# Optimization experiments

Hardware: AMD Instinct MI355X
Metric: run time of the kernel (lower is better)

Reference implementation:

```python
import jax, jax.numpy as jnp
import numpy as np

B, S, D, H = 2, 2048, 2048, 16
HD = D // H          # head_dim = 128
FF = 8192            # intermediate_size
LN_EPS = 1e-05
BIT_EPS = 1e-05


def _rope_tables(seq_len, head_dim):
    inv_freq = 1.0 / (10000.0 ** (np.arange(0, head_dim, 2, dtype=np.float64) / head_dim))
    ang = np.arange(seq_len, dtype=np.float64)[:, None] * inv_freq[None, :]  # [S, HD/2]
    ang = np.concatenate([ang, ang], axis=-1)  # [S, HD]
    return jnp.asarray(np.cos(ang), jnp.float32), jnp.asarray(np.sin(ang), jnp.float32)


def setup_inputs() -> dict:
    key = jax.random.key(0)
    ks = jax.random.split(key, 9)
    hidden_states = jax.random.normal(ks[0], (B, S, D), jnp.float32)
    # causal additive mask [1, S, S]
    causal = jnp.tril(jnp.ones((S, S), bool))
    attention_mask = jnp.where(causal, 0.0, -1e9)[None].astype(jnp.float32)
    cos, sin = _rope_tables(S, HD)
    w = lambda k, o, i: jax.random.normal(k, (o, i), jnp.float32) * 0.02
    return {
        'hidden_states': hidden_states,
        'attention_mask': attention_mask,
        'cos': cos, 'sin': sin,
        'wq': w(ks[1], D, D), 'wk': w(ks[2], D, D),
        'wv': w(ks[3], D, D), 'wo': w(ks[4], D, D),
        'wg': w(ks[5], FF, D), 'wu': w(ks[6], FF, D), 'wd': w(ks[7], D, FF),
        'ln1_w': jnp.ones((D,), jnp.float32),
        'ln2_w': jnp.ones((D,), jnp.float32),
    }


def bitlinear(x, w):
    # ternarize: clamp(round(w / (mean|w| + eps)), -1, 1); int8 cast in torch
    # breaks grad through the ternary values -> stop_gradient here.
    scale = jnp.mean(jnp.abs(w))
    tern = jax.lax.stop_gradient(jnp.clip(jnp.round(w / (scale + BIT_EPS)), -1.0, 1.0))
    # dequant = ternary * mean|w|, then standard linear (x @ W^T)
    return jnp.einsum('bsi,oi->bso', x, tern * scale)


def rmsnorm(x, w, eps=LN_EPS):
    var = jnp.mean(jnp.square(x.astype(jnp.float32)), axis=-1, keepdims=True)
    return w * (x * jax.lax.rsqrt(var + eps))


def rotate_half(x):
    x1, x2 = jnp.split(x, 2, axis=-1)
    return jnp.concatenate([-x2, x1], axis=-1)


def apply_rope(q, k, cos, sin):
    # q, k: [B, S, D] -> per-head rope -> back to [B, S, D]
    qh = q.reshape(B, S, H, HD)
    kh = k.reshape(B, S, H, HD)
    c = cos[None, :, None, :]
    s = sin[None, :, None, :]
    qe = qh * c + rotate_half(qh) * s
    ke = kh * c + rotate_half(kh) * s
    return qe.reshape(B, S, D), ke.reshape(B, S, D)


def reference(hidden_states, attention_mask, cos, sin,
              wq, wk, wv, wo, wg, wu, wd, ln1_w, ln2_w):
    residual = hidden_states
    # --- attention block ---
    x = rmsnorm(hidden_states, ln1_w)
    q = bitlinear(x, wq)
    k = bitlinear(x, wk)
    v = bitlinear(x, wv)
    q, k = apply_rope(q, k, cos, sin)
    # NOTE: scores over FULL hidden dim (no head split), scaled by sqrt(head_dim),
    # exactly as in the original module.
    scores = jnp.einsum('bsd,btd->bst', q, k) / jnp.sqrt(jnp.float32(HD))
    scores = scores + attention_mask
    probs = jax.nn.softmax(scores, axis=-1)
    attn_out = jnp.einsum('bst,btd->bsd', probs, v)
    attn_out = bitlinear(attn_out, wo)
    h = residual + attn_out
    # --- MLP block ---
    residual = h
    y = rmsnorm(h, ln2_w)
    gated = bitlinear(y, wg) * bitlinear(y, wu)
    out = bitlinear(gated, wd)
    return residual + out
```

## Files before the change

kernel.cpp:

```cpp
#include <hip/hip_runtime.h>
#include <stdint.h>

#define DEV __device__ __forceinline__

typedef __attribute__((ext_vector_type(8))) short short8;
typedef __attribute__((ext_vector_type(8))) __bf16 bf16x8;
typedef __attribute__((ext_vector_type(4))) float f32x4;

DEV unsigned short f2bf(float f) {
  union { float f; unsigned int u; } v; v.f = f;
  unsigned int r = v.u + 0x7fffu + ((v.u >> 16) & 1u);
  return (unsigned short)(r >> 16);
}
DEV float bf2f(unsigned short h) {
  union { unsigned int u; float f; } v; v.u = ((unsigned int)h) << 16;
  return v.f;
}
DEV f32x4 mfma16(short8 a, short8 b, f32x4 c) {
  return __builtin_amdgcn_mfma_f32_16x16x32_bf16(
      __builtin_bit_cast(bf16x8, a), __builtin_bit_cast(bf16x8, b), c, 0, 0, 0);
}
DEV void gload_lds16(const void* g, void* lds) {
  __builtin_amdgcn_global_load_lds(
      (const __attribute__((address_space(1))) void*)g,
      (__attribute__((address_space(3))) void*)lds, 16, 0, 0);
}

struct MArgs {
  const float* src[7];
  unsigned short* dst[7];
  int n[7];
  int sidx[7];
};

__global__ __launch_bounds__(256) void absmean_partial_multi(
    MArgs a, float* __restrict__ partial) {
  const int m = blockIdx.y;
  const float4* w4 = (const float4*)a.src[m];
  const int n4 = a.n[m] >> 2;
  float s = 0.f;
  for (int i = blockIdx.x * 256 + threadIdx.x; i < n4; i += 1024 * 256) {
    float4 v = w4[i];
    s += fabsf(v.x) + fabsf(v.y) + fabsf(v.z) + fabsf(v.w);
  }
#pragma unroll
  for (int mm = 1; mm < 64; mm <<= 1) s += __shfl_xor(s, mm);
  __shared__ float red[4];
  if ((threadIdx.x & 63) == 0) red[threadIdx.x >> 6] = s;
  __syncthreads();
  if (threadIdx.x == 0)
    partial[m * 1024 + blockIdx.x] = red[0] + red[1] + red[2] + red[3];
}

__global__ __launch_bounds__(256) void absmean_final(
    const float* __restrict__ partial, float* __restrict__ scales) {
  __shared__ double red[256];
  const int m = blockIdx.x;
  double s = 0.0;
  for (int i = threadIdx.x; i < 1024; i += 256) s += (double)partial[m * 1024 + i];
  red[threadIdx.x] = s;
  __syncthreads();
  for (int t = 128; t > 0; t >>= 1) {
    if (threadIdx.x < t) red[threadIdx.x] += red[threadIdx.x + t];
    __syncthreads();
  }
  if (threadIdx.x == 0) {
    const long long cnt = (m < 4) ? 4194304ll : 16777216ll;
    scales[m] = (float)(red[0] / (double)cnt);
  }
}

__global__ __launch_bounds__(256) void quantize_multi(
    MArgs a, const float* __restrict__ scales) {
  const int m = blockIdx.y;
  const float sc = scales[a.sidx[m]];
  const float inv = 1.f / (sc + 1e-5f);
  const float4* src = (const float4*)a.src[m];
  ushort4* dst = (ushort4*)a.dst[m];
  const int n4 = a.n[m] >> 2;
  for (int i = blockIdx.x * 256 + threadIdx.x; i < n4; i += 2048 * 256) {
    float4 v = src[i];
    ushort4 o;
    o.x = f2bf(fminf(fmaxf(rintf(v.x * inv), -1.f), 1.f) * sc);
    o.y = f2bf(fminf(fmaxf(rintf(v.y * inv), -1.f), 1.f) * sc);
    o.z = f2bf(fminf(fmaxf(rintf(v.z * inv), -1.f), 1.f) * sc);
    o.w = f2bf(fminf(fmaxf(rintf(v.w * inv), -1.f), 1.f) * sc);
    dst[i] = o;
  }
}

__global__ __launch_bounds__(256) void rmsnorm_k(
    const float* __restrict__ x, const float* __restrict__ wt,
    unsigned short* __restrict__ out) {
  const long long t = blockIdx.x;
  const float* xr = x + t * 2048;
  const int i0 = threadIdx.x * 8;
  float4 a = *(const float4*)(xr + i0);
  float4 b = *(const float4*)(xr + i0 + 4);
  float ss = a.x * a.x + a.y * a.y + a.z * a.z + a.w * a.w +
             b.x * b.x + b.y * b.y + b.z * b.z + b.w * b.w;
#pragma unroll
  for (int m = 1; m < 64; m <<= 1) ss += __shfl_xor(ss, m);
  __shared__ float red[4];
  if ((threadIdx.x & 63) == 0) red[threadIdx.x >> 6] = ss;
  __syncthreads();
  float tot = red[0] + red[1] + red[2] + red[3];
  float rs = rsqrtf(tot * (1.f / 2048.f) + 1e-5f);
  float4 wa = *(const float4*)(wt + i0);
  float4 wb = *(const float4*)(wt + i0 + 4);
  ushort4 o1, o2;
  o1.x = f2bf(a.x * wa.x * rs); o1.y = f2bf(a.y * wa.y * rs);
  o1.z = f2bf(a.z * wa.z * rs); o1.w = f2bf(a.w * wa.w * rs);
  o2.x = f2bf(b.x * wb.x * rs); o2.y = f2bf(b.y * wb.y * rs);
  o2.z = f2bf(b.z * wb.z * rs); o2.w = f2bf(b.w * wb.w * rs);
  *(ushort4*)(out + t * 2048 + i0) = o1;
  *(ushort4*)(out + t * 2048 + i0 + 4) = o2;
}

__global__ __launch_bounds__(256) void rope_k(
    const unsigned short* __restrict__ qkv, const float* __restrict__ cosT,
    const float* __restrict__ sinT, unsigned short* __restrict__ qr,
    unsigned short* __restrict__ kr, unsigned short* __restrict__ vt) {
  const long long gid = (long long)blockIdx.x * 256 + threadIdx.x;
  const int t = (int)(gid >> 10);
  const int r = (int)(gid & 1023);
  const int h = r >> 6, d = r & 63;
  const int s = t & 2047, b = t >> 11;
  const unsigned short* row = qkv + (long long)t * 6144;
  const float c = cosT[s * 128 + d], sn = sinT[s * 128 + d];
  const int col = h * 128 + d;
  const float SC = 0.08838834764831845f;
  float q1 = bf2f(row[col]), q2 = bf2f(row[col + 64]);
  float k1 = bf2f(row[2048 + col]), k2 = bf2f(row[2048 + col + 64]);
  long long ob = (long long)t * 2048 + col;
  qr[ob] = f2bf((q1 * c - q2 * sn) * SC);
  qr[ob + 64] = f2bf((q2 * c + q1 * sn) * SC);
  kr[ob] = f2bf(k1 * c - k2 * sn);
  kr[ob + 64] = f2bf(k2 * c + k1 * sn);
  vt[((long long)b * 2048 + col) * 2048 + s] = row[4096 + col];
  vt[((long long)b * 2048 + col + 64) * 2048 + s] = row[4096 + col + 64];
}

__global__ __launch_bounds__(256) void softmax_causal(
    const float* __restrict__ scores, unsigned short* __restrict__ probs) {
  const int r = blockIdx.x;
  const int s = r & 2047;
  const float* src = scores + (long long)r * 2048;
  unsigned short* dst = probs + (long long)r * 2048;
  const int L = s + 1;
  const int j0 = threadIdx.x * 8;
  float4 a = *(const float4*)(src + j0);
  float4 b = *(const float4*)(src + j0 + 4);
  float v[8] = {a.x, a.y, a.z, a.w, b.x, b.y, b.z, b.w};
  float mx = -1e30f;
#pragma unroll
  for (int i = 0; i < 8; ++i) {
    if (j0 + i >= L) v[i] = -1e30f;
    mx = fmaxf(mx, v[i]);
  }
#pragma unroll
  for (int m = 1; m < 64; m <<= 1) mx = fmaxf(mx, __shfl_xor(mx, m));
  __shared__ float redM[4], redS[4];
  if ((threadIdx.x & 63) == 0) redM[threadIdx.x >> 6] = mx;
  __syncthreads();
  mx = fmaxf(fmaxf(redM[0], redM[1]), fmaxf(redM[2], redM[3]));
  float sum = 0.f;
#pragma unroll
  for (int i = 0; i < 8; ++i) {
    v[i] = (j0 + i < L) ? __expf(v[i] - mx) : 0.f;
    sum += v[i];
  }
#pragma unroll
  for (int m = 1; m < 64; m <<= 1) sum += __shfl_xor(sum, m);
  if ((threadIdx.x & 63) == 0) redS[threadIdx.x >> 6] = sum;
  __syncthreads();
  const float inv = 1.f / (redS[0] + redS[1] + redS[2] + redS[3]);
  ushort4 o1, o2;
  o1.x = f2bf(v[0] * inv); o1.y = f2bf(v[1] * inv);
  o1.z = f2bf(v[2] * inv); o1.w = f2bf(v[3] * inv);
  o2.x = f2bf(v[4] * inv); o2.y = f2bf(v[5] * inv);
  o2.z = f2bf(v[6] * inv); o2.w = f2bf(v[7] * inv);
  *(ushort4*)(dst + j0) = o1;
  *(ushort4*)(dst + j0 + 4) = o2;
}

template <int EPI, int CAUSAL>
__global__ __launch_bounds__(512, 2) void gemm256(
    const unsigned short* __restrict__ A, const unsigned short* __restrict__ Bw,
    void* __restrict__ Cp, const void* __restrict__ Ep,
    int N, int K, int nbx, int kLen, int ngTot,
    long long sAz, long long sBz, long long zCout) {
  __shared__ __align__(16) unsigned short lds[4 * 2 * 8192];
  __shared__ __align__(16) unsigned short ldsDummy[512];
  const int tid = threadIdx.x;
  const int wid = tid >> 6, l = tid & 63;
  const int wr = wid >> 2, wcn = wid & 3;

  const int nwg = gridDim.x;
  const int q8 = nwg >> 3;
  const int lin = (blockIdx.x & 7) * q8 + (blockIdx.x >> 3);
  const int t32 = lin >> 5, r32 = lin & 31;
  const int tpr = nbx >> 3;
  const int tm = t32 / tpr, tn = t32 - tm * tpr;
  const long long m0 = (long long)(tm * 4 + (r32 >> 3)) * 256;
  const long long n0 = (long long)(tn * 8 + (r32 & 7)) * 256;
  if (CAUSAL == 1 && n0 > m0) return;
  const int z = blockIdx.z;
  A += z * sAz;
  Bw += z * sBz;
  const long long kbase = (long long)z * kLen;
  const long long zofs = (long long)z * zCout;
  int ng = ngTot;
  if (CAUSAL == 2) {
    const int lim = (int)((m0 + 256) >> 5);
    ng = lim < ng ? lim : ng;
  }

  const int stRow = (l >> 2);
  const int stCol = (((l & 3) ^ ((l >> 3) & 3))) * 8;
  auto stage = [&](int chunk) {
    if (chunk < ng) {
      char* base = (char*)lds + ((chunk & 3) * 2) * 16384;
      const long long kcol = kbase + (long long)chunk * 32 + stCol;
#pragma unroll
      for (int i = 0; i < 2; ++i) {
        const int row = (wid * 2 + i) * 16 + stRow;
        gload_lds16(&A[(m0 + row) * K + kcol], base + (wid * 2 + i) * 1024);
        gload_lds16(&Bw[(n0 + row) * K + kcol],
                    base + 16384 + (wid * 2 + i) * 1024);
      }
    } else {
#pragma unroll
      for (int i = 0; i < 4; ++i) gload_lds16(&A[m0 * K], (char*)ldsDummy);
    }
  };

  const int ar = l & 15;
  const int rj = ((l >> 4) ^ ((l >> 1) & 3)) << 4;

  auto readA03 = [&](int slot, short8 (&a)[4]) {
    const char* sA = (const char*)lds + (slot * 2) * 16384;
#pragma unroll
    for (int m = 0; m < 4; ++m)
      a[m] = *(const short8*)(sA + (wr * 128 + m * 16 + ar) * 64 + rj);
  };
  auto readA47 = [&](int slot, short8 (&a)[4]) {
    const char* sA = (const char*)lds + (slot * 2) * 16384;
#pragma unroll
    for (int m = 0; m < 4; ++m)
      a[m] = *(const short8*)(sA + (wr * 128 + (m + 4) * 16 + ar) * 64 + rj);
  };
  auto readB = [&](int slot, short8 (&b)[4]) {
    const char* sB = (const char*)lds + (slot * 2 + 1) * 16384;
#pragma unroll
    for (int n = 0; n < 4; ++n)
      b[n] = *(const short8*)(sB + (wcn * 64 + n * 16 + ar) * 64 + rj);
  };

  f32x4 acc[8][4] = {};
  short8 aX[4], bX[4], aY[4], bY[4], a47[4];

  stage(0); stage(1); stage(2);
  asm volatile("s_waitcnt vmcnt(4)" ::: "memory");
  __builtin_amdgcn_s_barrier();
  readA03(0, aX);
  readB(0, bX);

  auto chunkBody = [&](int c, bool sync, short8 (&cur03)[4], short8 (&curB)[4],
                       short8 (&nxt03)[4], short8 (&nxtB)[4]) {
    const int slot = c & 3;
    readA47(slot, a47);
    stage(c + 3);
    __builtin_amdgcn_s_setprio(1);
#pragma unroll
    for (int m = 0; m < 4; ++m)
#pragma unroll
      for (int n = 0; n < 4; ++n)
        acc[m][n] = mfma16(cur03[m], curB[n], acc[m][n]);
    __builtin_amdgcn_s_setprio(0);
    if (sync) {
      asm volatile("s_waitcnt vmcnt(4)" ::: "memory");
      __builtin_amdgcn_s_barrier();
    }
    readA03((c + 1) & 3, nxt03);
    readB((c + 1) & 3, nxtB);
    __builtin_amdgcn_s_setprio(1);
#pragma unroll
    for (int m = 0; m < 4; ++m)
#pragma unroll
      for (int n = 0; n < 4; ++n)
        acc[m + 4][n] = mfma16(a47[m], curB[n], acc[m + 4][n]);
    __builtin_amdgcn_s_setprio(0);
  };

  for (int c = 0; c < ng; c += 2) {
    chunkBody(c, false, aX, bX, aY, bY);
    chunkBody(c + 1, true, aY, bY, aX, bX);
  }
  asm volatile("s_waitcnt vmcnt(0)" ::: "memory");
  __builtin_amdgcn_s_barrier();

  const int orow = (l >> 4) * 4, ocol = l & 15;
#pragma unroll
  for (int m = 0; m < 8; ++m)
#pragma unroll
    for (int n = 0; n < 4; ++n)
#pragma unroll
      for (int r = 0; r < 4; ++r) {
        const long long gr = m0 + wr * 128 + m * 16 + orow + r;
        const long long gc = n0 + wcn * 64 + n * 16 + ocol;
        const long long idx = zofs + gr * N + gc;
        const float v = acc[m][n][r];
        if (EPI == 0) {
          ((unsigned short*)Cp)[idx] = f2bf(v);
        } else if (EPI == 2) {
          ((unsigned short*)Cp)[idx] = f2bf(bf2f(((const unsigned short*)Ep)[idx]) * v);
        } else {
          ((float*)Cp)[idx] = v;
        }
      }
}

__global__ __launch_bounds__(256) void combine2(
    const float* __restrict__ ep, const float* __restrict__ p,
    float* __restrict__ out, long long n4) {
  const float4* e4 = (const float4*)ep;
  const float4* p4 = (const float4*)p;
  float4* o4 = (float4*)out;
  for (long long i = blockIdx.x * 256 + threadIdx.x; i < n4; i += 2048 * 256) {
    float4 a = e4[i], b = p4[i], c = p4[i + n4];
    float4 o;
    o.x = a.x + b.x + c.x; o.y = a.y + b.y + c.y;
    o.z = a.z + b.z + c.z; o.w = a.w + b.w + c.w;
    o4[i] = o;
  }
}

extern "C" void kernel_launch(void* const* d_in, const int* in_sizes, int n_in,
                              void* d_out, int out_size, void* d_ws, size_t ws_size,
                              hipStream_t stream) {
  (void)in_sizes; (void)n_in; (void)out_size; (void)ws_size;
  const float* hidden = (const float*)d_in[0];
  const float* cosT = (const float*)d_in[2];
  const float* sinT = (const float*)d_in[3];
  const float* wq = (const float*)d_in[4];
  const float* wk = (const float*)d_in[5];
  const float* wv = (const float*)d_in[6];
  const float* wo = (const float*)d_in[7];
  const float* wg = (const float*)d_in[8];
  const float* wu = (const float*)d_in[9];
  const float* wd = (const float*)d_in[10];
  const float* ln1 = (const float*)d_in[11];
  const float* ln2 = (const float*)d_in[12];

  const size_t MB = 1ull << 20;
  char* ws = (char*)d_ws;
  unsigned short* xn    = (unsigned short*)(ws + 0);
  unsigned short* wqkvq = (unsigned short*)(ws + 16 * MB);
  unsigned short* qkv   = (unsigned short*)(ws + 40 * MB);
  unsigned short* qrb   = (unsigned short*)(ws + 88 * MB);
  unsigned short* krb   = (unsigned short*)(ws + 104 * MB);
  unsigned short* vtb   = (unsigned short*)(ws + 120 * MB);
  float*          scoresB = (float*)(ws + 0);
  unsigned short* probsB  = (unsigned short*)(ws + 40 * MB);
  float*          part   = (float*)(ws + 0);
  unsigned short* wgq   = (unsigned short*)(ws + 0);
  unsigned short* wuq   = (unsigned short*)(ws + 32 * MB);
  unsigned short* gbuf  = (unsigned short*)(ws + 64 * MB);
  unsigned short* attnb = (unsigned short*)(ws + 136 * MB);
  unsigned short* woq   = (unsigned short*)(ws + 152 * MB);
  float*          hbuf  = (float*)(ws + 160 * MB);
  unsigned short* ybuf  = (unsigned short*)(ws + 192 * MB);
  unsigned short* gated = (unsigned short*)(ws + 208 * MB);
  unsigned short* wdq   = (unsigned short*)(ws + 272 * MB);
  float* wspart         = (float*)(ws + 304 * MB);
  float* scales         = (float*)(ws + 304 * MB + 32768);

  MArgs am;
  am.src[0] = wq; am.src[1] = wk; am.src[2] = wv; am.src[3] = wo;
  am.src[4] = wg; am.src[5] = wu; am.src[6] = wd;
  am.n[0] = am.n[1] = am.n[2] = am.n[3] = 4194304;
  am.n[4] = am.n[5] = am.n[6] = 16777216;
  for (int i = 0; i < 7; ++i) { am.dst[i] = nullptr; am.sidx[i] = i; }
  absmean_partial_multi<<<dim3(1024, 7), 256, 0, stream>>>(am, wspart);
  absmean_final<<<7, 256, 0, stream>>>(wspart, scales);

  MArgs qe;
  qe.src[0] = wq; qe.dst[0] = wqkvq;            qe.n[0] = 4194304;  qe.sidx[0] = 0;
  qe.src[1] = wk; qe.dst[1] = wqkvq + 4194304;  qe.n[1] = 4194304;  qe.sidx[1] = 1;
  qe.src[2] = wv; qe.dst[2] = wqkvq + 8388608;  qe.n[2] = 4194304;  qe.sidx[2] = 2;
  qe.src[3] = wo; qe.dst[3] = woq;              qe.n[3] = 4194304;  qe.sidx[3] = 3;
  qe.src[4] = wd; qe.dst[4] = wdq;              qe.n[4] = 16777216; qe.sidx[4] = 6;
  qe.src[5] = wq; qe.dst[5] = nullptr; qe.n[5] = 0; qe.sidx[5] = 0;
  qe.src[6] = wq; qe.dst[6] = nullptr; qe.n[6] = 0; qe.sidx[6] = 0;
  quantize_multi<<<dim3(2048, 5), 256, 0, stream>>>(qe, scales);

  rmsnorm_k<<<4096, 256, 0, stream>>>(hidden, ln1, xn);

  gemm256<0, 0><<<dim3(384, 1, 1), 512, 0, stream>>>(
      xn, wqkvq, qkv, nullptr, 6144, 2048, 24, 2048, 64, 0, 0, 0);

  rope_k<<<16384, 256, 0, stream>>>(qkv, cosT, sinT, qrb, krb, vtb);

  gemm256<4, 1><<<dim3(64, 1, 2), 512, 0, stream>>>(
      qrb, krb, scoresB, nullptr, 2048, 2048, 8, 0, 64, 4194304, 4194304, 4194304);
  softmax_causal<<<4096, 256, 0, stream>>>(scoresB, probsB);
  gemm256<0, 2><<<dim3(64, 1, 2), 512, 0, stream>>>(
      probsB, vtb, attnb, nullptr, 2048, 2048, 8, 0, 64, 4194304, 4194304, 4194304);

  gemm256<4, 0><<<dim3(128, 1, 2), 512, 0, stream>>>(
      attnb, woq, part, nullptr, 2048, 2048, 8, 1024, 32, 0, 0, 8388608);
  combine2<<<2048, 256, 0, stream>>>(hidden, part, hbuf, 2097152);

  MArgs ql;
  ql.src[0] = wg; ql.dst[0] = wgq; ql.n[0] = 16777216; ql.sidx[0] = 4;
  ql.src[1] = wu; ql.dst[1] = wuq; ql.n[1] = 16777216; ql.sidx[1] = 5;
  for (int i = 2; i < 7; ++i) { ql.src[i] = wg; ql.dst[i] = nullptr; ql.n[i] = 0; ql.sidx[i] = 0; }
  quantize_multi<<<dim3(2048, 2), 256, 0, stream>>>(ql, scales);

  rmsnorm_k<<<4096, 256, 0, stream>>>(hbuf, ln2, ybuf);

  gemm256<0, 0><<<dim3(512, 1, 1), 512, 0, stream>>>(
      ybuf, wgq, gbuf, nullptr, 8192, 2048, 32, 2048, 64, 0, 0, 0);
  gemm256<2, 0><<<dim3(512, 1, 1), 512, 0, stream>>>(
      ybuf, wuq, gated, gbuf, 8192, 2048, 32, 2048, 64, 0, 0, 0);

  gemm256<4, 0><<<dim3(128, 1, 2), 512, 0, stream>>>(
      gated, wdq, part, nullptr, 2048, 8192, 8, 4096, 128, 0, 0, 8388608);
  combine2<<<2048, 256, 0, stream>>>(hbuf, part, (float*)d_out, 2097152);
}
```

Measured before the change: 824.8 us.

## Fuse residual combine with RMSNorm and unroll GEMM main loop by four

Replaces the separate split-K combine and second RMSNorm kernels with one kernel that sums the residual and both partials, writes h, and emits the normalized bf16 activations. This removes one launch and a re-read of the hidden buffer. The GEMM main loop is also unrolled four chunks deep so LDS slot indices and offsets become compile-time constants, which cuts address arithmetic. The unroll by four assumes ng is a multiple of four and raises code size and register pressure.

```diff
diff --git a/kernel.cpp b/kernel.cpp
--- a/kernel.cpp
+++ b/kernel.cpp
@@ -115,6 +115,48 @@
   o2.z = f2bf(b.z * wb.z * rs); o2.w = f2bf(b.w * wb.w * rs);
   *(ushort4*)(out + t * 2048 + i0) = o1;
   *(ushort4*)(out + t * 2048 + i0 + 4) = o2;
+}
+
+__global__ __launch_bounds__(256) void combine_rms(
+    const float* __restrict__ ep, const float* __restrict__ p,
+    const float* __restrict__ wt, float* __restrict__ hout,
+    unsigned short* __restrict__ yout) {
+  const long long t = blockIdx.x;
+  const int i0 = threadIdx.x * 8;
+  const long long base = t * 2048 + i0;
+  float4 e1 = *(const float4*)(ep + base);
+  float4 e2 = *(const float4*)(ep + base + 4);
+  float4 p1 = *(const float4*)(p + base);
+  float4 p2 = *(const float4*)(p + base + 4);
+  float4 q1 = *(const float4*)(p + 8388608 + base);
+  float4 q2 = *(const float4*)(p + 8388608 + base + 4);
+  float h[8] = {e1.x + p1.x + q1.x, e1.y + p1.y + q1.y,
+                e1.z + p1.z + q1.z, e1.w + p1.w + q1.w,
+                e2.x + p2.x + q2.x, e2.y + p2.y + q2.y,
+                e2.z + p2.z + q2.z, e2.w + p2.w + q2.w};
+  float4 h1 = {h[0], h[1], h[2], h[3]};
+  float4 h2 = {h[4], h[5], h[6], h[7]};
+  *(float4*)(hout + base) = h1;
+  *(float4*)(hout + base + 4) = h2;
+  float ss = 0.f;
+#pragma unroll
+  for (int i = 0; i < 8; ++i) ss += h[i] * h[i];
+#pragma unroll
+  for (int m = 1; m < 64; m <<= 1) ss += __shfl_xor(ss, m);
+  __shared__ float red[4];
+  if ((threadIdx.x & 63) == 0) red[threadIdx.x >> 6] = ss;
+  __syncthreads();
+  const float tot = red[0] + red[1] + red[2] + red[3];
+  const float rs = rsqrtf(tot * (1.f / 2048.f) + 1e-5f);
+  float4 wa = *(const float4*)(wt + i0);
+  float4 wb = *(const float4*)(wt + i0 + 4);
+  ushort4 o1, o2;
+  o1.x = f2bf(h[0] * wa.x * rs); o1.y = f2bf(h[1] * wa.y * rs);
+  o1.z = f2bf(h[2] * wa.z * rs); o1.w = f2bf(h[3] * wa.w * rs);
+  o2.x = f2bf(h[4] * wb.x * rs); o2.y = f2bf(h[5] * wb.y * rs);
+  o2.z = f2bf(h[6] * wb.z * rs); o2.w = f2bf(h[7] * wb.w * rs);
+  *(ushort4*)(yout + base) = o1;
+  *(ushort4*)(yout + base + 4) = o2;
 }
 
 __global__ __launch_bounds__(256) void rope_k(
@@ -218,9 +260,9 @@
 
   const int stRow = (l >> 2);
   const int stCol = (((l & 3) ^ ((l >> 3) & 3))) * 8;
-  auto stage = [&](int chunk) {
+  auto stage = [&](int chunk, int sslot) {
     if (chunk < ng) {
-      char* base = (char*)lds + ((chunk & 3) * 2) * 16384;
+      char* base = (char*)lds + (sslot * 2) * 16384;
       const long long kcol = kbase + (long long)chunk * 32 + stCol;
 #pragma unroll
       for (int i = 0; i < 2; ++i) {
@@ -237,66 +279,58 @@
 
   const int ar = l & 15;
   const int rj = ((l >> 4) ^ ((l >> 1) & 3)) << 4;
-
-  auto readA03 = [&](int slot, short8 (&a)[4]) {
-    const char* sA = (const char*)lds + (slot * 2) * 16384;
-#pragma unroll
-    for (int m = 0; m < 4; ++m)
-      a[m] = *(const short8*)(sA + (wr * 128 + m * 16 + ar) * 64 + rj);
-  };
-  auto readA47 = [&](int slot, short8 (&a)[4]) {
-    const char* sA = (const char*)lds + (slot * 2) * 16384;
-#pragma unroll
-    for (int m = 0; m < 4; ++m)
-      a[m] = *(const short8*)(sA + (wr * 128 + (m + 4) * 16 + ar) * 64 + rj);
-  };
-  auto readB = [&](int slot, short8 (&b)[4]) {
-    const char* sB = (const char*)lds + (slot * 2 + 1) * 16384;
-#pragma unroll
-    for (int n = 0; n < 4; ++n)
-      b[n] = *(const short8*)(sB + (wcn * 64 + n * 16 + ar) * 64 + rj);
-  };
+  const int aoff = (wr * 128 + ar) * 64 + rj;
+  const int boff = (wcn * 64 + ar) * 64 + rj;
 
   f32x4 acc[8][4] = {};
-  short8 aX[4], bX[4], aY[4], bY[4], a47[4];
-
-  stage(0); stage(1); stage(2);
+  short8 aX[4], bX[4], aY[4], bY[4];
+
+  stage(0, 0); stage(1, 1); stage(2, 2);
   asm volatile("s_waitcnt vmcnt(4)" ::: "memory");
   __builtin_amdgcn_s_barrier();
-  readA03(0, aX);
-  readB(0, bX);
-
-  auto chunkBody = [&](int c, bool sync, short8 (&cur03)[4], short8 (&curB)[4],
-                       short8 (&nxt03)[4], short8 (&nxtB)[4]) {
-    const int slot = c & 3;
-    readA47(slot, a47);
-    stage(c + 3);
-    __builtin_amdgcn_s_setprio(1);
-#pragma unroll
-    for (int m = 0; m < 4; ++m)
-#pragma unroll
-      for (int n = 0; n < 4; ++n)
-        acc[m][n] = mfma16(cur03[m], curB[n], acc[m][n]);
-    __builtin_amdgcn_s_setprio(0);
-    if (sync) {
-      asm volatile("s_waitcnt vmcnt(4)" ::: "memory");
-      __builtin_amdgcn_s_barrier();
-    }
-    readA03((c + 1) & 3, nxt03);
-    readB((c + 1) & 3, nxtB);
-    __builtin_amdgcn_s_setprio(1);
-#pragma unroll
-    for (int m = 0; m < 4; ++m)
-#pragma unroll
-      for (int n = 0; n < 4; ++n)
-        acc[m + 4][n] = mfma16(a47[m], curB[n], acc[m + 4][n]);
-    __builtin_amdgcn_s_setprio(0);
-  };
-
-  for (int c = 0; c < ng; c += 2) {
-    chunkBody(c, false, aX, bX, aY, bY);
-    chunkBody(c + 1, true, aY, bY, aX, bX);
-  }
+#pragma unroll
+  for (int m = 0; m < 4; ++m)
+    aX[m] = *(const short8*)((const char*)lds + aoff + m * 1024);
+#pragma unroll
+  for (int n = 0; n < 4; ++n)
+    bX[n] = *(const short8*)((const char*)lds + 16384 + boff + n * 1024);
+
+#define CHUNK_BODY(SLOT, NSLOT, SYNC, cur03, curB, nxt03, nxtB, cc)            \
+  {                                                                            \
+    const char* sAc = (const char*)lds + (SLOT * 2) * 16384;                   \
+    const char* sAn = (const char*)lds + (NSLOT * 2) * 16384;                  \
+    const char* sBn = (const char*)lds + (NSLOT * 2 + 1) * 16384;              \
+    short8 a47[4];                                                             \
+    _Pragma("unroll") for (int m = 0; m < 4; ++m)                              \
+        a47[m] = *(const short8*)(sAc + aoff + 4096 + m * 1024);               \
+    stage((cc) + 3, (SLOT + 3) & 3);                                           \
+    __builtin_amdgcn_s_setprio(1);                                             \
+    _Pragma("unroll") for (int m = 0; m < 4; ++m)                              \
+      _Pragma("unroll") for (int n = 0; n < 4; ++n)                            \
+          acc[m][n] = mfma16(cur03[m], curB[n], acc[m][n]);                    \
+    __builtin_amdgcn_s_setprio(0);                                             \
+    if (SYNC) {                                                                \
+      asm volatile("s_waitcnt vmcnt(4)" ::: "memory");                         \
+      __builtin_amdgcn_s_barrier();                                            \
+    }                                                                          \
+    _Pragma("unroll") for (int m = 0; m < 4; ++m)                              \
+        nxt03[m] = *(const short8*)(sAn + aoff + m * 1024);                    \
+    _Pragma("unroll") for (int n = 0; n < 4; ++n)                              \
+        nxtB[n] = *(const short8*)(sBn + boff + n * 1024);                     \
+    __builtin_amdgcn_s_setprio(1);                                             \
+    _Pragma("unroll") for (int m = 0; m < 4; ++m)                              \
+      _Pragma("unroll") for (int n = 0; n < 4; ++n)                            \
+          acc[m + 4][n] = mfma16(a47[m], curB[n], acc[m + 4][n]);              \
+    __builtin_amdgcn_s_setprio(0);                                             \
+  }
+
+  for (int c = 0; c < ng; c += 4) {
+    CHUNK_BODY(0, 1, false, aX, bX, aY, bY, c);
+    CHUNK_BODY(1, 2, true, aY, bY, aX, bX, c + 1);
+    CHUNK_BODY(2, 3, false, aX, bX, aY, bY, c + 2);
+    CHUNK_BODY(3, 0, true, aY, bY, aX, bX, c + 3);
+  }
+#undef CHUNK_BODY
   asm volatile("s_waitcnt vmcnt(0)" ::: "memory");
   __builtin_amdgcn_s_barrier();
 
@@ -410,7 +444,7 @@
 
   gemm256<4, 0><<<dim3(128, 1, 2), 512, 0, stream>>>(
       attnb, woq, part, nullptr, 2048, 2048, 8, 1024, 32, 0, 0, 8388608);
-  combine2<<<2048, 256, 0, stream>>>(hidden, part, hbuf, 2097152);
+  combine_rms<<<4096, 256, 0, stream>>>(hidden, part, ln2, hbuf, ybuf);
 
   MArgs ql;
   ql.src[0] = wg; ql.dst[0] = wgq; ql.n[0] = 16777216; ql.sidx[0] = 4;
@@ -418,8 +452,6 @@
   for (int i = 2; i < 7; ++i) { ql.src[i] = wg; ql.dst[i] = nullptr; ql.n[i] = 0; ql.sidx[i] = 0; }
   quantize_multi<<<dim3(2048, 2), 256, 0, stream>>>(ql, scales);
 
-  rmsnorm_k<<<4096, 256, 0, stream>>>(hbuf, ln2, ybuf);
-
   gemm256<0, 0><<<dim3(512, 1, 1), 512, 0, stream>>>(
       ybuf, wgq, gbuf, nullptr, 8192, 2048, 32, 2048, 64, 0, 0, 0);
   gemm256<2, 0><<<dim3(512, 1, 1), 512, 0, stream>>>(
```

Result: no change. 818.8 us (-0.7%).
